# Optimization experiments

Hardware: AMD Instinct MI355X
Metric: run time of the kernel (lower is better)

The kernel has to match this reference:

```python
import jax, jax.numpy as jnp
import numpy as np

N = 50000
E = 800000
N_CT = 32
EMBED = 256
HIDDEN = 128
OUT = 512
NEG_SLOPE = 0.2


def setup_inputs() -> dict:
    key = jax.random.key(0)
    ks = jax.random.split(key, 12)
    ct_idx = jax.random.randint(ks[0], (N,), 0, N_CT)
    cell_type_onehot = jax.nn.one_hot(ct_idx, N_CT, dtype=jnp.float32)
    lipid_droplet_scalar = jax.random.normal(ks[1], (N,), dtype=jnp.float32)
    edge_index = jax.random.randint(ks[2], (2, E), 0, N, dtype=jnp.int32)
    s = 0.05
    return {
        "cell_type_onehot": cell_type_onehot,
        "lipid_droplet_scalar": lipid_droplet_scalar,
        "edge_index": edge_index,
        "W_embed": jax.random.normal(ks[3], (N_CT + 1, EMBED), dtype=jnp.float32) * s,
        "b_embed": jnp.zeros((EMBED,), dtype=jnp.float32),
        "W_l": jax.random.normal(ks[4], (EMBED, HIDDEN), dtype=jnp.float32) * s,
        "b_l": jnp.zeros((HIDDEN,), dtype=jnp.float32),
        "W_r": jax.random.normal(ks[5], (EMBED, HIDDEN), dtype=jnp.float32) * s,
        "b_r": jnp.zeros((HIDDEN,), dtype=jnp.float32),
        "att": jax.random.normal(ks[6], (HIDDEN,), dtype=jnp.float32) * s,
        "gat_bias": jnp.zeros((HIDDEN,), dtype=jnp.float32),
        "W_out": jax.random.normal(ks[7], (HIDDEN, OUT), dtype=jnp.float32) * s,
        "b_out": jnp.zeros((OUT,), dtype=jnp.float32),
        "dispersion": jax.random.normal(ks[8], (OUT, N_CT), dtype=jnp.float32) * s,
    }


def reference(cell_type_onehot, lipid_droplet_scalar, edge_index,
              W_embed, b_embed, W_l, b_l, W_r, b_r, att, gat_bias,
              W_out, b_out, dispersion):
    n = cell_type_onehot.shape[0]
    lds = lipid_droplet_scalar[:, None] if lipid_droplet_scalar.ndim == 1 else lipid_droplet_scalar
    combined = jnp.concatenate([cell_type_onehot, lds], axis=1)  # [N, n_ct+1]
    x = jax.nn.elu(combined @ W_embed + b_embed)  # [N, EMBED]

    # GATv2Conv, heads=1, concat=True (PyG semantics)
    x_l = x @ W_l + b_l  # source-side transform [N, H]
    x_r = x @ W_r + b_r  # target-side transform [N, H]
    src, dst = edge_index[0], edge_index[1]
    e = jax.nn.leaky_relu(x_l[src] + x_r[dst], negative_slope=NEG_SLOPE)  # [E, H]
    logit = e @ att  # [E]
    # scatter-softmax over incoming edges of each target node
    m = jax.ops.segment_max(logit, dst, num_segments=n)
    alpha = jnp.exp(logit - m[dst])
    denom = jax.ops.segment_sum(alpha, dst, num_segments=n)
    alpha = alpha / (denom[dst] + 1e-16)
    agg = jax.ops.segment_sum(alpha[:, None] * x_l[src], dst, num_segments=n)  # [N, H]
    h = jax.nn.elu(agg + gat_bias)

    logits = h @ W_out + b_out  # [N, OUT]
    ct_idx = jnp.argmax(cell_type_onehot, axis=1)  # [N]
    disp = jax.nn.softplus(dispersion[:, ct_idx]).T  # [N, OUT]
    return logits, disp
```

## Files before the change

### kernel.cpp

```cpp
#include <hip/hip_runtime.h>
#include <hip/hip_bf16.h>
#include <math.h>

#define N    50000
#define E    800000
#define NCT  32
#define EMB  256
#define HID  128
#define OUTD 512
#define NB_SCAN 49
#define XPAD 260

__device__ __forceinline__ float4 fma4s(float a, float4 b, float4 c) {
    return make_float4(fmaf(a, b.x, c.x), fmaf(a, b.y, c.y),
                       fmaf(a, b.z, c.z), fmaf(a, b.w, c.w));
}
__device__ __forceinline__ float4 add4(float4 a, float4 b) {
    return make_float4(a.x + b.x, a.y + b.y, a.z + b.z, a.w + b.w);
}

__global__ void k_init(const float* __restrict__ onehot,
                       const float* __restrict__ dispersion,
                       int* __restrict__ ct, int* __restrict__ hist,
                       float* __restrict__ spt) {
    int i = blockIdx.x * 256 + threadIdx.x;
    if (i < N) {
        const float* row = onehot + (size_t)i * NCT;
        int c = 0;
        #pragma unroll
        for (int j = 0; j < NCT; j++)
            if (row[j] > 0.5f) c = j;
        ct[i] = c;
        hist[i] = 0;
    }
    if (i < OUTD * NCT) {
        float x = dispersion[i];
        float s = log1pf(expf(-fabsf(x))) + fmaxf(x, 0.f);
        int c = i >> 5, j = i & 31;
        spt[j * OUTD + c] = s;
    }
}

__global__ __launch_bounds__(256) void k_hist(const int* __restrict__ eidx,
                                              int* __restrict__ hist) {
    int i = blockIdx.x * 256 + threadIdx.x;
    if (i < E / 4) {
        int4 d = reinterpret_cast<const int4*>(eidx + E)[i];
        atomicAdd(&hist[d.x], 1);
        atomicAdd(&hist[d.y], 1);
        atomicAdd(&hist[d.z], 1);
        atomicAdd(&hist[d.w], 1);
    }
}

__global__ __launch_bounds__(256, 2) void k_xlr(
        const int* __restrict__ ct, const float* __restrict__ ldsc,
        const float* __restrict__ We, const float* __restrict__ be,
        const float* __restrict__ pWl, const float* __restrict__ pbl,
        const float* __restrict__ pWr, const float* __restrict__ pbr,
        float* __restrict__ xl, float* __restrict__ xr) {
    __shared__ float xs[64 * XPAD];
    __shared__ float Bs[16 * HID];
    __shared__ int   ctl[64];
    __shared__ float ldl[64];
    const int t    = threadIdx.x;
    const int b    = blockIdx.x & 1;
    const int n0   = (blockIdx.x >> 1) * 64;

    if (t < 64) {
        int n = n0 + t; if (n >= N) n = N - 1;
        ctl[t] = ct[n];
        ldl[t] = ldsc[n];
    }
    __syncthreads();

    {
        const float w32 = We[NCT * EMB + t];
        const float bb  = be[t];
        for (int m = 0; m < 64; m++) {
            float v = fmaf(ldl[m], w32, We[ctl[m] * EMB + t]) + bb;
            xs[m * XPAD + t] = v > 0.f ? v : expm1f(v);
        }
    }

    const float* W  = b ? pWr : pbl == pbr ? pWr : pWl;
    const float* Wp = b ? pWr : pWl;
    (void)W;
    const int rg = t >> 5;
    const int cg = t & 31;
    const int c  = cg * 4;
    const float* xrow = xs + rg * 8 * XPAD;
    const int st_kk  = t >> 5;
    const int st_col = (t & 31) * 4;

    float4 acc[8];
    #pragma unroll
    for (int r = 0; r < 8; r++) acc[r] = make_float4(0.f, 0.f, 0.f, 0.f);

    for (int kc = 0; kc < EMB; kc += 16) {
        __syncthreads();
        *reinterpret_cast<float4*>(&Bs[st_kk * HID + st_col]) =
            *reinterpret_cast<const float4*>(Wp + (size_t)(kc + st_kk) * HID + st_col);
        *reinterpret_cast<float4*>(&Bs[(st_kk + 8) * HID + st_col]) =
            *reinterpret_cast<const float4*>(Wp + (size_t)(kc + st_kk + 8) * HID + st_col);
        __syncthreads();

        #pragma unroll
        for (int kk = 0; kk < 16; kk += 4) {
            float4 bq[4];
            #pragma unroll
            for (int q = 0; q < 4; q++)
                bq[q] = *reinterpret_cast<const float4*>(&Bs[(kk + q) * HID + c]);
            float4 a[8];
            #pragma unroll
            for (int r = 0; r < 8; r++)
                a[r] = *reinterpret_cast<const float4*>(xrow + r * XPAD + kc + kk);
            #pragma unroll
            for (int r = 0; r < 8; r++) {
                acc[r] = fma4s(a[r].x, bq[0], acc[r]);
                acc[r] = fma4s(a[r].y, bq[1], acc[r]);
                acc[r] = fma4s(a[r].z, bq[2], acc[r]);
                acc[r] = fma4s(a[r].w, bq[3], acc[r]);
            }
        }
    }

    float* outP = b ? xr : xl;
    const float4 bias = *reinterpret_cast<const float4*>((b ? pbr : pbl) + c);
    #pragma unroll
    for (int r = 0; r < 8; r++) {
        int n = n0 + rg * 8 + r;
        if (n < N)
            *reinterpret_cast<float4*>(outP + (size_t)n * HID + c) = add4(acc[r], bias);
    }
}

__global__ __launch_bounds__(1024) void k_scan1(const int* __restrict__ hist,
                                                int* __restrict__ offs,
                                                int* __restrict__ bsum) {
    __shared__ int sb[2][1024];
    const int t = threadIdx.x;
    const int i = blockIdx.x * 1024 + t;
    int v = (i < N) ? hist[i] : 0;
    sb[0][t] = v;
    __syncthreads();
    int pin = 0;
    for (int off = 1; off < 1024; off <<= 1) {
        int x = sb[pin][t];
        if (t >= off) x += sb[pin][t - off];
        sb[pin ^ 1][t] = x;
        pin ^= 1;
        __syncthreads();
    }
    int incl = sb[pin][t];
    if (i < N) offs[i] = incl - v;
    if (t == 1023) bsum[blockIdx.x] = incl;
}

__global__ void k_scan2(const int* __restrict__ bsum, int* __restrict__ bbase) {
    if (threadIdx.x == 0) {
        int run = 0;
        for (int j = 0; j < NB_SCAN; j++) { bbase[j] = run; run += bsum[j]; }
    }
}

__global__ __launch_bounds__(1024) void k_scan3(int* __restrict__ offs,
                                                int* __restrict__ cursor,
                                                const int* __restrict__ bbase) {
    const int t = threadIdx.x;
    const int i = blockIdx.x * 1024 + t;
    if (i < N) {
        int v = offs[i] + bbase[blockIdx.x];
        offs[i] = v;
        cursor[i] = v;
    }
    if (blockIdx.x == 0 && t == 0) offs[N] = E;
}

__global__ __launch_bounds__(256) void k_scatter(const int* __restrict__ eidx,
                                                 int* __restrict__ cursor,
                                                 int* __restrict__ sorted) {
    const int e = blockIdx.x * 256 + threadIdx.x;
    if (e < E) {
        int s = eidx[e];
        int d = eidx[E + e];
        int pos = atomicAdd(&cursor[d], 1);
        sorted[pos] = s;
    }
}

__global__ __launch_bounds__(256, 8) void k_agg(
        const int* __restrict__ offs, const int* __restrict__ srt,
        const float* __restrict__ xl, const float* __restrict__ attv,
        const float* __restrict__ gb, float* xrh) {
    const int t = threadIdx.x;
    const int n = blockIdx.x * 8 + (t >> 5);
    if (n >= N) return;
    const int lane = t & 31;
    const float4* xl4 = reinterpret_cast<const float4*>(xl);
    float4* xh4 = reinterpret_cast<float4*>(xrh);

    const float4 xr4 = xh4[(size_t)n * 32 + lane];
    const float4 at4 = reinterpret_cast<const float4*>(attv)[lane];
    const int i0  = offs[n];
    const int deg = offs[n + 1] - i0;

    float m = -3.0e38f, den = 0.f;
    float4 acc = make_float4(0.f, 0.f, 0.f, 0.f);

#define STEP(XC) {                                                          \
    float vx = XC.x + xr4.x, vy = XC.y + xr4.y,                             \
          vz = XC.z + xr4.z, vw = XC.w + xr4.w;                             \
    vx = fmaxf(vx, 0.f) + 0.2f * fminf(vx, 0.f);                            \
    vy = fmaxf(vy, 0.f) + 0.2f * fminf(vy, 0.f);                            \
    vz = fmaxf(vz, 0.f) + 0.2f * fminf(vz, 0.f);                            \
    vw = fmaxf(vw, 0.f) + 0.2f * fminf(vw, 0.f);                            \
    float p = fmaf(vx, at4.x, fmaf(vy, at4.y, fmaf(vz, at4.z, vw * at4.w)));\
    p += __shfl_xor(p, 16); p += __shfl_xor(p, 8);                          \
    p += __shfl_xor(p, 4);  p += __shfl_xor(p, 2); p += __shfl_xor(p, 1);   \
    float mn = fmaxf(m, p);                                                 \
    float sc = __expf(m - mn);                                              \
    float w  = __expf(p - mn);                                              \
    den   = fmaf(den, sc, w);                                               \
    acc.x = fmaf(acc.x, sc, w * XC.x);                                      \
    acc.y = fmaf(acc.y, sc, w * XC.y);                                      \
    acc.z = fmaf(acc.z, sc, w * XC.z);                                      \
    acc.w = fmaf(acc.w, sc, w * XC.w);                                      \
    m = mn; }

    if (deg > 0) {
        const int lastI = i0 + deg - 1;
        #define LDX(J) xl4[(size_t)srt[min(i0 + (J), lastI)] * 32 + lane]
        float4 x0 = LDX(0), x1 = LDX(1), x2 = LDX(2), x3 = LDX(3);
        int i = 0;
        for (; i + 4 <= deg; i += 4) {
            const int base = i0 + i + 4;
            float4 n0 = xl4[(size_t)srt[min(base + 0, lastI)] * 32 + lane];
            float4 n1 = xl4[(size_t)srt[min(base + 1, lastI)] * 32 + lane];
            float4 n2 = xl4[(size_t)srt[min(base + 2, lastI)] * 32 + lane];
            float4 n3 = xl4[(size_t)srt[min(base + 3, lastI)] * 32 + lane];
            STEP(x0); STEP(x1); STEP(x2); STEP(x3);
            x0 = n0; x1 = n1; x2 = n2; x3 = n3;
        }
        if (i     < deg) STEP(x0);
        if (i + 1 < deg) STEP(x1);
        if (i + 2 < deg) STEP(x2);
        #undef LDX
    }
#undef STEP

    float inv = 1.f / (den + 1e-16f);
    const float4 g4 = reinterpret_cast<const float4*>(gb)[lane];
    float hx = fmaf(acc.x, inv, g4.x);
    float hy = fmaf(acc.y, inv, g4.y);
    float hz = fmaf(acc.z, inv, g4.z);
    float hw = fmaf(acc.w, inv, g4.w);
    hx = hx > 0.f ? hx : expm1f(hx);
    hy = hy > 0.f ? hy : expm1f(hy);
    hz = hz > 0.f ? hz : expm1f(hz);
    hw = hw > 0.f ? hw : expm1f(hw);
    xh4[(size_t)n * 32 + lane] = make_float4(hx, hy, hz, hw);
}

__global__ __launch_bounds__(256, 3) void k_out(
        const float* __restrict__ h, const int* __restrict__ ct,
        const float* __restrict__ Wo, const float* __restrict__ bo,
        const float* __restrict__ spt, float* __restrict__ out) {
    __shared__ float hs[32 * HID];
    __shared__ float Bs[16 * OUTD];
    __shared__ int ctl[32];
    const int t  = threadIdx.x;
    const int n0 = blockIdx.x * 32;

    if (t < 32) { int n = n0 + t; ctl[t] = ct[n < N ? n : N - 1]; }
    {
        const float4* h4 = reinterpret_cast<const float4*>(h);
        #pragma unroll
        for (int j = 0; j < 4; j++) {
            int fi  = t + j * 256;
            int row = fi >> 5;
            int k4  = (fi & 31) * 4;
            int n = n0 + row;
            float4 v = (n < N) ? h4[(size_t)n * 32 + (fi & 31)]
                               : make_float4(0.f, 0.f, 0.f, 0.f);
            *reinterpret_cast<float4*>(&hs[row * HID + k4]) = v;
        }
    }

    const int rg = t >> 6;
    const int cg = t & 63;
    const int c0 = cg * 4;
    const int c1 = 256 + cg * 4;
    const float* hrow = hs + rg * 8 * HID;
    const int st_kk  = t >> 7;
    const int st_col = (t & 127) * 4;

    float4 acc0[8], acc1[8];
    #pragma unroll
    for (int r = 0; r < 8; r++) {
        acc0[r] = make_float4(0.f, 0.f, 0.f, 0.f);
        acc1[r] = make_float4(0.f, 0.f, 0.f, 0.f);
    }

    for (int kc = 0; kc < HID; kc += 16) {
        __syncthreads();
        #pragma unroll
        for (int j = 0; j < 8; j++) {
            int kk = st_kk + j * 2;
            *reinterpret_cast<float4*>(&Bs[kk * OUTD + st_col]) =
                *reinterpret_cast<const float4*>(Wo + (size_t)(kc + kk) * OUTD + st_col);
        }
        __syncthreads();

        #pragma unroll
        for (int kk = 0; kk < 16; kk += 4) {
            float4 a[8];
            #pragma unroll
            for (int r = 0; r < 8; r++)
                a[r] = *reinterpret_cast<const float4*>(hrow + r * HID + kc + kk);
            #pragma unroll
            for (int q = 0; q < 4; q++) {
                float4 b0 = *reinterpret_cast<const float4*>(&Bs[(kk + q) * OUTD + c0]);
                float4 b1 = *reinterpret_cast<const float4*>(&Bs[(kk + q) * OUTD + c1]);
                const float* aq = reinterpret_cast<const float*>(a);
                #pragma unroll
                for (int r = 0; r < 8; r++) {
                    float av = aq[r * 4 + q];
                    acc0[r] = fma4s(av, b0, acc0[r]);
                    acc1[r] = fma4s(av, b1, acc1[r]);
                }
            }
        }
    }

    float* outd = out + (size_t)N * OUTD;
    const float4 bias0 = *reinterpret_cast<const float4*>(bo + c0);
    const float4 bias1 = *reinterpret_cast<const float4*>(bo + c1);
    #pragma unroll
    for (int r = 0; r < 8; r++) {
        int row = rg * 8 + r;
        int n = n0 + row;
        if (n < N) {
            *reinterpret_cast<float4*>(out + (size_t)n * OUTD + c0) = add4(acc0[r], bias0);
            *reinterpret_cast<float4*>(out + (size_t)n * OUTD + c1) = add4(acc1[r], bias1);
            int cn = ctl[row];
            *reinterpret_cast<float4*>(outd + (size_t)n * OUTD + c0) =
                *reinterpret_cast<const float4*>(spt + cn * OUTD + c0);
            *reinterpret_cast<float4*>(outd + (size_t)n * OUTD + c1) =
                *reinterpret_cast<const float4*>(spt + cn * OUTD + c1);
        }
    }
}

extern "C" void kernel_launch(void* const* d_in, const int* in_sizes, int n_in,
                              void* d_out, int out_size, void* d_ws, size_t ws_size,
                              hipStream_t stream) {
    const float* onehot     = (const float*)d_in[0];
    const float* ldsc       = (const float*)d_in[1];
    const int*   eidx       = (const int*)  d_in[2];
    const float* We         = (const float*)d_in[3];
    const float* be         = (const float*)d_in[4];
    const float* Wl         = (const float*)d_in[5];
    const float* bl         = (const float*)d_in[6];
    const float* Wr         = (const float*)d_in[7];
    const float* br         = (const float*)d_in[8];
    const float* attv       = (const float*)d_in[9];
    const float* gb         = (const float*)d_in[10];
    const float* Wo         = (const float*)d_in[11];
    const float* bo         = (const float*)d_in[12];
    const float* dispersion = (const float*)d_in[13];

    float* ws     = (float*)d_ws;
    float* xl     = ws;
    float* xr     = xl + (size_t)N * HID;
    int*   sorted = (int*)(xr + (size_t)N * HID);
    int*   ct     = sorted + E;
    int*   offs   = ct + N;
    int*   cursor = offs + (N + 1);
    int*   hist   = cursor + (N + 1);
    float* spt    = (float*)(hist + N);
    int*   bsum   = (int*)(spt + NCT * OUTD);
    int*   bbase  = bsum + 64;

    float* out = (float*)d_out;

    const int xlr_tiles = (N + 63) / 64;

    k_init   <<<(N + 255) / 256, 256, 0, stream>>>(onehot, dispersion, ct, hist, spt);
    k_hist   <<<(E / 4 + 255) / 256, 256, 0, stream>>>(eidx, hist);
    k_xlr    <<<xlr_tiles * 2, 256, 0, stream>>>(ct, ldsc, We, be, Wl, bl, Wr, br, xl, xr);
    k_scan1  <<<NB_SCAN, 1024, 0, stream>>>(hist, offs, bsum);
    k_scan2  <<<1, 64, 0, stream>>>(bsum, bbase);
    k_scan3  <<<NB_SCAN, 1024, 0, stream>>>(offs, cursor, bbase);
    k_scatter<<<(E + 255) / 256, 256, 0, stream>>>(eidx, cursor, sorted);
    k_agg    <<<(N + 7) / 8, 256, 0, stream>>>(offs, sorted, xl, attv, gb, xr);
    k_out    <<<(N + 31) / 32, 256, 0, stream>>>(xr, ct, Wo, bo, spt, out);
}
```

Measured before the change: 578.4 us.

## Split embedding into separate kernel and double-buffer weight tiles in xlr GEMM

Moves the ELU embedding computation out of the xl/xr GEMM into its own elementwise kernel that writes x to global workspace. The GEMM then reads A operands directly from global/L2 instead of a large LDS tile, which frees LDS so occupancy can rise (launch bounds 2 -> 4). Weight tiles are widened to 32 rows and double-buffered to halve barrier count. It adds a 51MB write plus reads of x through global memory, and uncoalesced per-thread float4 row reads in the GEMM.

After: 660.3 us. 1.14x slower.

```diff
diff --git a/kernel.cpp b/kernel.cpp
--- a/kernel.cpp
+++ b/kernel.cpp
@@ -9,7 +9,6 @@
 #define HID  128
 #define OUTD 512
 #define NB_SCAN 49
-#define XPAD 260
 
 __device__ __forceinline__ float4 fma4s(float a, float4 b, float4 c) {
     return make_float4(fmaf(a, b.x, c.x), fmaf(a, b.y, c.y),
@@ -41,6 +40,31 @@
     }
 }
 
+__global__ __launch_bounds__(256) void k_embed(
+        const int* __restrict__ ct, const float* __restrict__ ldsc,
+        const float* __restrict__ We, const float* __restrict__ be,
+        float* __restrict__ x) {
+    int gid = blockIdx.x * 256 + threadIdx.x;
+    if (gid >= N * (EMB / 4)) return;
+    int n  = gid >> 6;
+    int d  = (gid & 63) * 4;
+    int c  = ct[n];
+    float l = ldsc[n];
+    float4 wc  = *reinterpret_cast<const float4*>(We + (size_t)c * EMB + d);
+    float4 w32 = *reinterpret_cast<const float4*>(We + (size_t)NCT * EMB + d);
+    float4 bb  = *reinterpret_cast<const float4*>(be + d);
+    float4 v;
+    v.x = fmaf(l, w32.x, wc.x) + bb.x;
+    v.y = fmaf(l, w32.y, wc.y) + bb.y;
+    v.z = fmaf(l, w32.z, wc.z) + bb.z;
+    v.w = fmaf(l, w32.w, wc.w) + bb.w;
+    v.x = v.x > 0.f ? v.x : expm1f(v.x);
+    v.y = v.y > 0.f ? v.y : expm1f(v.y);
+    v.z = v.z > 0.f ? v.z : expm1f(v.z);
+    v.w = v.w > 0.f ? v.w : expm1f(v.w);
+    *reinterpret_cast<float4*>(x + (size_t)n * EMB + d) = v;
+}
+
 __global__ __launch_bounds__(256) void k_hist(const int* __restrict__ eidx,
                                               int* __restrict__ hist) {
     int i = blockIdx.x * 256 + threadIdx.x;
@@ -53,43 +77,27 @@
     }
 }
 
-__global__ __launch_bounds__(256, 2) void k_xlr(
-        const int* __restrict__ ct, const float* __restrict__ ldsc,
-        const float* __restrict__ We, const float* __restrict__ be,
+__global__ __launch_bounds__(256, 4) void k_xlr(
+        const float* __restrict__ x,
         const float* __restrict__ pWl, const float* __restrict__ pbl,
         const float* __restrict__ pWr, const float* __restrict__ pbr,
         float* __restrict__ xl, float* __restrict__ xr) {
-    __shared__ float xs[64 * XPAD];
-    __shared__ float Bs[16 * HID];
-    __shared__ int   ctl[64];
-    __shared__ float ldl[64];
-    const int t    = threadIdx.x;
-    const int b    = blockIdx.x & 1;
-    const int n0   = (blockIdx.x >> 1) * 64;
-
-    if (t < 64) {
-        int n = n0 + t; if (n >= N) n = N - 1;
-        ctl[t] = ct[n];
-        ldl[t] = ldsc[n];
-    }
-    __syncthreads();
-
-    {
-        const float w32 = We[NCT * EMB + t];
-        const float bb  = be[t];
-        for (int m = 0; m < 64; m++) {
-            float v = fmaf(ldl[m], w32, We[ctl[m] * EMB + t]) + bb;
-            xs[m * XPAD + t] = v > 0.f ? v : expm1f(v);
-        }
-    }
-
-    const float* W  = b ? pWr : pbl == pbr ? pWr : pWl;
+    __shared__ float Bs[2][32 * HID];
+    const int t  = threadIdx.x;
+    const int b  = blockIdx.x & 1;
+    const int n0 = (blockIdx.x >> 1) * 64;
     const float* Wp = b ? pWr : pWl;
-    (void)W;
+
     const int rg = t >> 5;
     const int cg = t & 31;
     const int c  = cg * 4;
-    const float* xrow = xs + rg * 8 * XPAD;
+    const int row0 = n0 + rg * 8;
+    const float* xrow[8];
+    #pragma unroll
+    for (int r = 0; r < 8; r++) {
+        int n = row0 + r; if (n >= N) n = N - 1;
+        xrow[r] = x + (size_t)n * EMB;
+    }
     const int st_kk  = t >> 5;
     const int st_col = (t & 31) * 4;
 
@@ -97,24 +105,34 @@
     #pragma unroll
     for (int r = 0; r < 8; r++) acc[r] = make_float4(0.f, 0.f, 0.f, 0.f);
 
-    for (int kc = 0; kc < EMB; kc += 16) {
-        __syncthreads();
-        *reinterpret_cast<float4*>(&Bs[st_kk * HID + st_col]) =
-            *reinterpret_cast<const float4*>(Wp + (size_t)(kc + st_kk) * HID + st_col);
-        *reinterpret_cast<float4*>(&Bs[(st_kk + 8) * HID + st_col]) =
-            *reinterpret_cast<const float4*>(Wp + (size_t)(kc + st_kk + 8) * HID + st_col);
-        __syncthreads();
-
+    #pragma unroll
+    for (int j = 0; j < 4; j++) {
+        int kk = st_kk + j * 8;
+        *reinterpret_cast<float4*>(&Bs[0][kk * HID + st_col]) =
+            *reinterpret_cast<const float4*>(Wp + (size_t)kk * HID + st_col);
+    }
+    __syncthreads();
+
+    for (int kc = 0; kc < EMB; kc += 32) {
+        const int cur = (kc >> 5) & 1;
+        if (kc + 32 < EMB) {
+            #pragma unroll
+            for (int j = 0; j < 4; j++) {
+                int kk = st_kk + j * 8;
+                *reinterpret_cast<float4*>(&Bs[cur ^ 1][kk * HID + st_col]) =
+                    *reinterpret_cast<const float4*>(Wp + (size_t)(kc + 32 + kk) * HID + st_col);
+            }
+        }
         #pragma unroll
-        for (int kk = 0; kk < 16; kk += 4) {
+        for (int kk = 0; kk < 32; kk += 4) {
             float4 bq[4];
             #pragma unroll
             for (int q = 0; q < 4; q++)
-                bq[q] = *reinterpret_cast<const float4*>(&Bs[(kk + q) * HID + c]);
+                bq[q] = *reinterpret_cast<const float4*>(&Bs[cur][(kk + q) * HID + c]);
             float4 a[8];
             #pragma unroll
             for (int r = 0; r < 8; r++)
-                a[r] = *reinterpret_cast<const float4*>(xrow + r * XPAD + kc + kk);
+                a[r] = *reinterpret_cast<const float4*>(xrow[r] + kc + kk);
             #pragma unroll
             for (int r = 0; r < 8; r++) {
                 acc[r] = fma4s(a[r].x, bq[0], acc[r]);
@@ -123,13 +141,14 @@
                 acc[r] = fma4s(a[r].w, bq[3], acc[r]);
             }
         }
+        __syncthreads();
     }
 
     float* outP = b ? xr : xl;
     const float4 bias = *reinterpret_cast<const float4*>((b ? pbr : pbl) + c);
     #pragma unroll
     for (int r = 0; r < 8; r++) {
-        int n = n0 + rg * 8 + r;
+        int n = row0 + r;
         if (n < N)
             *reinterpret_cast<float4*>(outP + (size_t)n * HID + c) = add4(acc[r], bias);
     }
@@ -381,14 +400,16 @@
     float* spt    = (float*)(hist + N);
     int*   bsum   = (int*)(spt + NCT * OUTD);
     int*   bbase  = bsum + 64;
+    float* x      = (float*)(bbase + 64);
 
     float* out = (float*)d_out;
 
     const int xlr_tiles = (N + 63) / 64;
 
     k_init   <<<(N + 255) / 256, 256, 0, stream>>>(onehot, dispersion, ct, hist, spt);
+    k_embed  <<<(N * (EMB / 4) + 255) / 256, 256, 0, stream>>>(ct, ldsc, We, be, x);
     k_hist   <<<(E / 4 + 255) / 256, 256, 0, stream>>>(eidx, hist);
-    k_xlr    <<<xlr_tiles * 2, 256, 0, stream>>>(ct, ldsc, We, be, Wl, bl, Wr, br, xl, xr);
+    k_xlr    <<<xlr_tiles * 2, 256, 0, stream>>>(x, Wl, bl, Wr, br, xl, xr);
     k_scan1  <<<NB_SCAN, 1024, 0, stream>>>(hist, offs, bsum);
     k_scan2  <<<1, 64, 0, stream>>>(bsum, bbase);
     k_scan3  <<<NB_SCAN, 1024, 0, stream>>>(offs, cursor, bbase);
```
